# Performance work log

Hardware: AMD Instinct MI355X
Metric: run time of the kernel (lower is better)

## Reference

```python
import math
import jax, jax.numpy as jnp
import numpy as np

B, S, D, H, P, FF = 64, 100, 768, 8, 8, 3072
HD = D // H
NUM_LAYERS = 4
EPS = 1e-5


def _layernorm(x, g, b):
    m = jnp.mean(x, axis=-1, keepdims=True)
    v = jnp.mean(jnp.square(x - m), axis=-1, keepdims=True)
    return (x - m) * jax.lax.rsqrt(v + EPS) * g + b


def _positional_encoding(seq_len, d_model):
    pos = jnp.arange(seq_len, dtype=jnp.float32)[:, None]
    div = jnp.exp(jnp.arange(0, d_model, 2, dtype=jnp.float32) * (-math.log(10000.0) / d_model))
    pe = jnp.zeros((seq_len, d_model), dtype=jnp.float32)
    pe = pe.at[:, 0::2].set(jnp.sin(pos * div))
    pe = pe.at[:, 1::2].set(jnp.cos(pos * div))
    return pe[None]  # [1, S, D]


def setup_inputs() -> dict:
    key = jax.random.key(0)
    ks = jax.random.split(key, 12)
    s = 0.02
    return {
        "template_seq": jax.random.normal(ks[0], (B, S, D), jnp.float32),
        "param_seq": jax.random.normal(ks[1], (B, S, P, 768), jnp.float32),
        # ParamEncoder (shared across all 4 layers)
        "Wc": jax.random.normal(ks[2], (768, D), jnp.float32) * s,
        "bc": jnp.zeros((D,), jnp.float32),
        "gp": jnp.ones((D,), jnp.float32),
        "bp": jnp.zeros((D,), jnp.float32),
        # FFN (shared)
        "W1": jax.random.normal(ks[3], (D, FF), jnp.float32) * s,
        "b1": jnp.zeros((FF,), jnp.float32),
        "W2": jax.random.normal(ks[4], (FF, D), jnp.float32) * s,
        "b2": jnp.zeros((D,), jnp.float32),
        # LayerNorms (shared)
        "g1": jnp.ones((D,), jnp.float32),
        "bn1": jnp.zeros((D,), jnp.float32),
        "g2": jnp.ones((D,), jnp.float32),
        "bn2": jnp.zeros((D,), jnp.float32),
        # final classifier
        "Wfc": jax.random.normal(ks[5], (D * S, 2), jnp.float32) * s,
        "bfc": jnp.zeros((2,), jnp.float32),
    }


def _layer(src, param_seq, Wc, bc, gp, bp, W1, b1, W2, b2, g1, bn1, g2, bn2):
    inv_sqrt_hd = 1.0 / math.sqrt(HD)
    # ParamEncoder: Linear(768->D) per param vector, mean over params, LayerNorm.
    # Linear is linear => mean-then-project is identical to project-then-mean.
    pooled = jnp.mean(param_seq, axis=2)                  # [B, S, 768]
    param_enc = _layernorm(pooled @ Wc + bc, gp, bp)       # [B, S, D]
    pb = param_enc.reshape(B, S, H, HD).transpose(0, 2, 1, 3)  # [B, H, S, HD]
    param_bias = jnp.einsum('bhqd,bhkd->bhqk', pb, pb) * inv_sqrt_hd
    # attention with q = k = v = src (no projections in the original forward)
    q = src.reshape(B, S, H, HD).transpose(0, 2, 1, 3)     # [B, H, S, HD]
    attn = jnp.einsum('bhqd,bhkd->bhqk', q, q) * inv_sqrt_hd + param_bias
    attn = jax.nn.softmax(attn, axis=-1)
    out = jnp.einsum('bhqk,bhkd->bhqd', attn, q)
    out = out.transpose(0, 2, 1, 3).reshape(B, S, D)
    src = _layernorm(src + out, g1, bn1)
    ffn = jax.nn.gelu(src @ W1 + b1, approximate=False) @ W2 + b2
    return _layernorm(src + ffn, g2, bn2)


def reference(template_seq, param_seq, Wc, bc, gp, bp, W1, b1, W2, b2,
              g1, bn1, g2, bn2, Wfc, bfc):
    x = template_seq + _positional_encoding(S, D)
    for _ in range(NUM_LAYERS):
        x = _layer(x, param_seq, Wc, bc, gp, bp, W1, b1, W2, b2, g1, bn1, g2, bn2)
    return x.reshape(B, S * D) @ Wfc + bfc  # [B, 2]
```

## Files before the change

### kernel.cpp

```cpp
#include <hip/hip_runtime.h>
#include <hip/hip_bf16.h>
#include <math.h>


typedef __attribute__((ext_vector_type(8))) short bf16x8;
typedef __attribute__((ext_vector_type(4))) float f32x4;
typedef __attribute__((ext_vector_type(4))) short short4v;

#define BB 64
#define SS 100
#define DD 768
#define HH 8
#define HD 96
#define FF_ 3072
#define ROWS 6400
#define LN10000 9.210340371976184f

__device__ __forceinline__ void async_copy16(void* lds_dst, const void* gsrc) {
  __builtin_amdgcn_global_load_lds(
      (const __attribute__((address_space(1))) void*)gsrc,
      (__attribute__((address_space(3))) void*)lds_dst, 16, 0, 0);
}

__device__ __forceinline__ float block_sum256(float v, float* sbuf) {
#pragma unroll
  for (int o = 32; o > 0; o >>= 1) v += __shfl_xor(v, o, 64);
  int tid = threadIdx.x;
  __syncthreads();
  if ((tid & 63) == 0) sbuf[tid >> 6] = v;
  __syncthreads();
  return sbuf[0] + sbuf[1] + sbuf[2] + sbuf[3];
}

__device__ __forceinline__ float block_sum192(float v, float* sbuf) {
#pragma unroll
  for (int o = 32; o > 0; o >>= 1) v += __shfl_xor(v, o, 64);
  int tid = threadIdx.x;
  __syncthreads();
  if ((tid & 63) == 0) sbuf[tid >> 6] = v;
  __syncthreads();
  return sbuf[0] + sbuf[1] + sbuf[2];
}

__global__ void convert_transpose(const float* __restrict__ in,
                                  __hip_bfloat16* __restrict__ out,
                                  int K, int N) {
  __shared__ float t[32][33];
  int n0 = blockIdx.x * 32, k0 = blockIdx.y * 32;
  int tid = threadIdx.x;
  int tx = tid & 31, ty = tid >> 5;
#pragma unroll
  for (int j = 0; j < 32; j += 8)
    t[ty + j][tx] = in[(size_t)(k0 + ty + j) * N + n0 + tx];
  __syncthreads();
#pragma unroll
  for (int j = 0; j < 32; j += 8)
    out[(size_t)(n0 + ty + j) * K + k0 + tx] = __float2bfloat16(t[tx][ty + j]);
}

__global__ void pool_mean(const float* __restrict__ ps,
                          __hip_bfloat16* __restrict__ pooled) {
  int idx = blockIdx.x * 256 + threadIdx.x;
  int row = idx / DD, c = idx - row * DD;
  float s = 0.f;
#pragma unroll
  for (int p = 0; p < 8; p++) s += ps[(size_t)(row * 8 + p) * DD + c];
  pooled[idx] = __float2bfloat16(s * 0.125f);
}

__global__ void add_pe(const float* __restrict__ t, float* __restrict__ src) {
  int idx = blockIdx.x * 256 + threadIdx.x;
  int row = idx / DD, c = idx - row * DD;
  int srow = row % SS;
  int c2 = c & ~1;
  float ang = (float)srow * expf((float)c2 * (-LN10000 / (float)DD));
  float pe = (c & 1) ? cosf(ang) : sinf(ang);
  src[idx] = t[idx] + pe;
}

template <bool XB16, bool RESID, bool WB16>
__global__ void ln_row(const float* __restrict__ Xf,
                       const __hip_bfloat16* __restrict__ Xb,
                       const float* __restrict__ R,
                       const float* __restrict__ g, const float* __restrict__ bb,
                       float* __restrict__ of, __hip_bfloat16* __restrict__ ob) {
  int row = blockIdx.x, tid = threadIdx.x;
  size_t base = (size_t)row * DD;
  int c4 = tid * 4;
  float4 v;
  if constexpr (XB16) {
    short4v xv = *(const short4v*)(Xb + base + c4);
    __hip_bfloat16* p = (__hip_bfloat16*)&xv;
    v.x = __bfloat162float(p[0]); v.y = __bfloat162float(p[1]);
    v.z = __bfloat162float(p[2]); v.w = __bfloat162float(p[3]);
  } else {
    v = *(const float4*)(Xf + base + c4);
  }
  if (RESID) {
    float4 rv = *(const float4*)(R + base + c4);
    v.x += rv.x; v.y += rv.y; v.z += rv.z; v.w += rv.w;
  }
  __shared__ float sbuf[3];
  float s = block_sum192(v.x + v.y + v.z + v.w, sbuf);
  float mean = s * (1.0f / DD);
  float dx = v.x - mean, dy = v.y - mean, dz = v.z - mean, dw = v.w - mean;
  float ss = block_sum192(dx * dx + dy * dy + dz * dz + dw * dw, sbuf);
  float rs = rsqrtf(ss * (1.0f / DD) + 1e-5f);
  float4 gv = *(const float4*)(g + c4);
  float4 bv = *(const float4*)(bb + c4);
  float4 y;
  y.x = dx * rs * gv.x + bv.x;
  y.y = dy * rs * gv.y + bv.y;
  y.z = dz * rs * gv.z + bv.z;
  y.w = dw * rs * gv.w + bv.w;
  *(float4*)(of + base + c4) = y;
  if (WB16) {
    __hip_bfloat16 hb[4] = {__float2bfloat16(y.x), __float2bfloat16(y.y),
                            __float2bfloat16(y.z), __float2bfloat16(y.w)};
    *(short4v*)(ob + base + c4) = *(short4v*)hb;
  }
}

__launch_bounds__(256, 2)
__global__ void param_bias_mfma(const float* __restrict__ penc,
                                float* __restrict__ pbias) {
  __shared__ __align__(16) __hip_bfloat16 Qs[128][104];
  const int bh = blockIdx.x;
  const int b = bh >> 3, h = bh & 7;
  const int tid = threadIdx.x;
  const int wave = tid >> 6, lane = tid & 63;
  const int r = lane & 15, quad = lane >> 4;
  const int q8 = quad * 8;
  const int wr = (wave >> 1) * 64, wc = (wave & 1) * 64;
  const float sroot = rsqrtf(9.79795897113f);
  for (int i = tid; i < 128 * HD; i += 256) {
    int s = i / HD, d = i - s * HD;
    float v = (s < SS) ? penc[(size_t)(b * SS + s) * DD + h * HD + d] : 0.f;
    Qs[s][d] = __float2bfloat16(v * sroot);
  }
  __syncthreads();
  f32x4 acc[4][4] = {};
#pragma unroll
  for (int k0 = 0; k0 < HD; k0 += 32) {
    bf16x8 af[4], bfv[4];
#pragma unroll
    for (int mi = 0; mi < 4; mi++)
      af[mi] = *(const bf16x8*)&Qs[wr + mi * 16 + r][k0 + q8];
#pragma unroll
    for (int ni = 0; ni < 4; ni++)
      bfv[ni] = *(const bf16x8*)&Qs[wc + ni * 16 + r][k0 + q8];
#pragma unroll
    for (int mi = 0; mi < 4; mi++)
#pragma unroll
      for (int ni = 0; ni < 4; ni++)
        acc[mi][ni] = __builtin_amdgcn_mfma_f32_16x16x32_bf16(af[mi], bfv[ni],
                                                              acc[mi][ni], 0, 0, 0);
  }
  float* pb = pbias + (size_t)bh * SS * SS;
#pragma unroll
  for (int mi = 0; mi < 4; mi++)
#pragma unroll
    for (int ni = 0; ni < 4; ni++) {
      int col = wc + ni * 16 + r;
      if (col < SS) {
#pragma unroll
        for (int rg = 0; rg < 4; rg++) {
          int row = wr + mi * 16 + quad * 4 + rg;
          if (row < SS) pb[row * SS + col] = acc[mi][ni][rg];
        }
      }
    }
}

__launch_bounds__(256, 2)
__global__ void attn_fused_mfma(const float* __restrict__ src,
                                const float* __restrict__ pbias,
                                __hip_bfloat16* __restrict__ out) {
  __shared__ __align__(16) char umem[128 * 136 * 2];
  __shared__ __align__(16) __hip_bfloat16 Qt[96][136];
  __shared__ float redm[2][128];
  __shared__ float reds[2][128];
  __hip_bfloat16 (*Qs)[104] = (__hip_bfloat16 (*)[104])umem;
  __hip_bfloat16 (*Ps)[136] = (__hip_bfloat16 (*)[136])umem;

  const int bh = blockIdx.x;
  const int b = bh >> 3, h = bh & 7;
  const int tid = threadIdx.x;
  const int wave = tid >> 6, lane = tid & 63;
  const int r = lane & 15, quad = lane >> 4;
  const int q8 = quad * 8;
  const int wr = (wave >> 1) * 64, wc = (wave & 1) * 64;

  const float sroot = rsqrtf(9.79795897113f);
  for (int i = tid; i < SS * HD; i += 256) {
    int s = i / HD, d = i - s * HD;
    float v = src[(size_t)(b * SS + s) * DD + h * HD + d];
    Qs[s][d] = __float2bfloat16(v * sroot);
    Qt[d][s] = __float2bfloat16(v);
  }
  for (int i = tid; i < 28 * HD; i += 256) {
    int s = i / HD, d = i - s * HD;
    Qs[100 + s][d] = __float2bfloat16(0.f);
    Qt[d][100 + s] = __float2bfloat16(0.f);
  }

  const float* pb = pbias + (size_t)bh * SS * SS;
  bool cv[4]; int cols[4];
#pragma unroll
  for (int ni = 0; ni < 4; ni++) { cols[ni] = wc + ni * 16 + r; cv[ni] = cols[ni] < SS; }
  f32x4 acc[4][4];
#pragma unroll
  for (int mi = 0; mi < 4; mi++)
#pragma unroll
    for (int rg = 0; rg < 4; rg++) {
      int row = wr + mi * 16 + quad * 4 + rg;
#pragma unroll
      for (int ni = 0; ni < 4; ni++)
        acc[mi][ni][rg] = (row < SS && cv[ni]) ? pb[row * SS + cols[ni]] : 0.f;
    }
  __syncthreads();

#pragma unroll
  for (int k0 = 0; k0 < HD; k0 += 32) {
    bf16x8 af[4], bfv[4];
#pragma unroll
    for (int mi = 0; mi < 4; mi++)
      af[mi] = *(const bf16x8*)&Qs[wr + mi * 16 + r][k0 + q8];
#pragma unroll
    for (int ni = 0; ni < 4; ni++)
      bfv[ni] = *(const bf16x8*)&Qs[wc + ni * 16 + r][k0 + q8];
#pragma unroll
    for (int mi = 0; mi < 4; mi++)
#pragma unroll
      for (int ni = 0; ni < 4; ni++)
        acc[mi][ni] = __builtin_amdgcn_mfma_f32_16x16x32_bf16(af[mi], bfv[ni],
                                                              acc[mi][ni], 0, 0, 0);
  }

  float mx[4][4];
#pragma unroll
  for (int mi = 0; mi < 4; mi++)
#pragma unroll
    for (int rg = 0; rg < 4; rg++) {
      float m = -1e30f;
#pragma unroll
      for (int ni = 0; ni < 4; ni++)
        if (cv[ni]) m = fmaxf(m, acc[mi][ni][rg]);
#pragma unroll
      for (int o = 1; o < 16; o <<= 1) m = fmaxf(m, __shfl_xor(m, o, 64));
      mx[mi][rg] = m;
    }
  if (r == 0) {
#pragma unroll
    for (int mi = 0; mi < 4; mi++)
#pragma unroll
      for (int rg = 0; rg < 4; rg++)
        redm[wave & 1][wr + mi * 16 + quad * 4 + rg] = mx[mi][rg];
  }
  __syncthreads();

#pragma unroll
  for (int mi = 0; mi < 4; mi++)
#pragma unroll
    for (int rg = 0; rg < 4; rg++) {
      int row = wr + mi * 16 + quad * 4 + rg;
      float rmax = fmaxf(redm[0][row], redm[1][row]);
      float s = 0.f;
#pragma unroll
      for (int ni = 0; ni < 4; ni++) {
        float e = cv[ni] ? __expf(acc[mi][ni][rg] - rmax) : 0.f;
        acc[mi][ni][rg] = e;
        s += e;
      }
#pragma unroll
      for (int o = 1; o < 16; o <<= 1) s += __shfl_xor(s, o, 64);
      if (r == 0) reds[wave & 1][row] = s;
    }
  __syncthreads();

#pragma unroll
  for (int mi = 0; mi < 4; mi++)
#pragma unroll
    for (int rg = 0; rg < 4; rg++) {
      int row = wr + mi * 16 + quad * 4 + rg;
      float inv = 1.0f / (reds[0][row] + reds[1][row]);
#pragma unroll
      for (int ni = 0; ni < 4; ni++)
        Ps[row][cols[ni]] = __float2bfloat16(acc[mi][ni][rg] * inv);
    }
  __syncthreads();

  const int wr2 = (wave >> 1) * 48;
  f32x4 po[3][4] = {};
#pragma unroll
  for (int kk = 0; kk < 128; kk += 32) {
    bf16x8 aq[3], bp[4];
#pragma unroll
    for (int mi = 0; mi < 3; mi++)
      aq[mi] = *(const bf16x8*)&Qt[wr2 + mi * 16 + r][kk + q8];
#pragma unroll
    for (int ni = 0; ni < 4; ni++)
      bp[ni] = *(const bf16x8*)&Ps[wc + ni * 16 + r][kk + q8];
#pragma unroll
    for (int mi = 0; mi < 3; mi++)
#pragma unroll
      for (int ni = 0; ni < 4; ni++)
        po[mi][ni] = __builtin_amdgcn_mfma_f32_16x16x32_bf16(aq[mi], bp[ni],
                                                             po[mi][ni], 0, 0, 0);
  }
#pragma unroll
  for (int mi = 0; mi < 3; mi++)
#pragma unroll
    for (int ni = 0; ni < 4; ni++) {
      int qcol = wc + ni * 16 + r;
      if (qcol < SS) {
        int d0 = wr2 + mi * 16 + quad * 4;
        __hip_bfloat16 hb[4];
#pragma unroll
        for (int rg = 0; rg < 4; rg++) hb[rg] = __float2bfloat16(po[mi][ni][rg]);
        *(short4v*)(out + (size_t)(b * SS + qcol) * DD + h * HD + d0) = *(short4v*)hb;
      }
    }
}

template <int MODE>
__launch_bounds__(512, 4)
__global__ void gemm256(const __hip_bfloat16* __restrict__ A,
                        const __hip_bfloat16* __restrict__ Bt,
                        const float* __restrict__ bias,
                        const float* __restrict__ resid,
                        float* __restrict__ outf,
                        __hip_bfloat16* __restrict__ outb,
                        int M, int N, int K) {
  constexpr int BM = 256, BN = 128, BK = 32;
  __shared__ __align__(16) __hip_bfloat16 As[3][BM * BK];
  __shared__ __align__(16) __hip_bfloat16 Bs[3][BN * BK];
  const int gm = M >> 8, gn = N >> 7;
  const int nwg = gm * gn;
  int wg = (int)blockIdx.x;
  {
    int qc = nwg >> 3, rc = nwg & 7;
    int xcd = wg & 7, pos = wg >> 3;
    wg = (xcd < rc ? xcd * (qc + 1) : rc * (qc + 1) + (xcd - rc) * qc) + pos;
  }
  const int nt0 = wg / gm, mt = wg - nt0 * gm;
  const int m0 = mt * BM, n0 = nt0 * BN;
  const int tid = threadIdx.x;
  const int wave = tid >> 6, lane = tid & 63;
  const int wm = wave >> 1, wn = wave & 1;
  const int r = lane & 15, q = lane >> 4;

  const int srow = tid >> 2;
  const int scp = (tid & 3) ^ ((srow >> 1) & 3);
  const __hip_bfloat16* gA0 = A + (size_t)(m0 + srow) * K + scp * 8;
  const __hip_bfloat16* gA1 = A + (size_t)(m0 + srow + 128) * K + scp * 8;
  const __hip_bfloat16* gB0 = Bt + (size_t)(n0 + srow) * K + scp * 8;

  const int key8 = ((r >> 1) & 3) * 8;
  const int cq = (q * 8) ^ key8;
  const int aBase = wm * 2048 + r * 32;
  const int bBase = wn * 2048 + r * 32;

  f32x4 acc[4][4] = {};

  const int NT = K / BK;
#pragma unroll
  for (int t = 0; t < 2; ++t) {
    const int kel = t * BK;
    async_copy16(&As[t][tid * 8],          gA0 + kel);
    async_copy16(&As[t][(tid + 512) * 8],  gA1 + kel);
    async_copy16(&Bs[t][tid * 8],          gB0 + kel);
  }
  asm volatile("s_waitcnt vmcnt(3)" ::: "memory");
  __builtin_amdgcn_s_barrier();
  __builtin_amdgcn_sched_barrier(0);

  int slot = 0;
  for (int t = 0; t < NT; ++t) {
    const int s2 = (slot >= 1) ? slot - 1 : slot + 2;
    const bool st = (t + 2 < NT);
    const int kel = (t + 2) * BK;
    bf16x8 af[4], bfr[4];
#pragma unroll
    for (int mi = 0; mi < 4; mi++)
      af[mi] = *(const bf16x8*)(&As[slot][aBase + mi * 512 + cq]);
#pragma unroll
    for (int ni = 0; ni < 4; ni++)
      bfr[ni] = *(const bf16x8*)(&Bs[slot][bBase + ni * 512 + cq]);
    if (st) {
      async_copy16(&As[s2][tid * 8],         gA0 + kel);
      async_copy16(&As[s2][(tid + 512) * 8], gA1 + kel);
      async_copy16(&Bs[s2][tid * 8],         gB0 + kel);
    }
    __builtin_amdgcn_s_setprio(1);
#pragma unroll
    for (int mi = 0; mi < 4; mi++)
#pragma unroll
      for (int ni = 0; ni < 4; ni++)
        acc[mi][ni] = __builtin_amdgcn_mfma_f32_16x16x32_bf16(af[mi], bfr[ni],
                                                              acc[mi][ni], 0, 0, 0);
    __builtin_amdgcn_s_setprio(0);
    if (st) asm volatile("s_waitcnt vmcnt(3)" ::: "memory");
    else    asm volatile("s_waitcnt vmcnt(0)" ::: "memory");
    __builtin_amdgcn_s_barrier();
    __builtin_amdgcn_sched_barrier(0);
    slot = (slot == 2) ? 0 : slot + 1;
  }

#pragma unroll
  for (int mi = 0; mi < 4; mi++) {
#pragma unroll
    for (int ni = 0; ni < 4; ni++) {
      int col = n0 + wn * 64 + ni * 16 + r;
      float bv = bias[col];
#pragma unroll
      for (int rg = 0; rg < 4; rg++) {
        int row = m0 + wm * 64 + mi * 16 + q * 4 + rg;
        size_t oidx = (size_t)row * N + col;
        float v = acc[mi][ni][rg] + bv;
        if constexpr (MODE == 2) v += resid[oidx];
        if constexpr (MODE == 1) {
          v = 0.5f * v * (1.0f + erff(v * 0.70710678118654752f));
          outb[oidx] = __float2bfloat16(v);
        } else {
          outf[oidx] = v;
        }
      }
    }
  }
}

#define CCHUNK 3072
#define NCHUNK 25
__global__ void classifier_part(const float* __restrict__ x,
                                const float* __restrict__ Wfc,
                                float* __restrict__ part) {
  int chunk = blockIdx.x, b = blockIdx.y, tid = threadIdx.x;
  const float* xb = x + (size_t)b * (SS * DD) + chunk * CCHUNK;
  const float* w = Wfc + 2 * (size_t)chunk * CCHUNK;
  float a0 = 0.f, a1 = 0.f;
  for (int i = tid; i < CCHUNK; i += 256) {
    float xv = xb[i];
    float2 wv = *(const float2*)(w + 2 * i);
    a0 += xv * wv.x;
    a1 += xv * wv.y;
  }
  __shared__ float sbuf[4];
  a0 = block_sum256(a0, sbuf);
  a1 = block_sum256(a1, sbuf);
  if (tid == 0) {
    part[(b * NCHUNK + chunk) * 2] = a0;
    part[(b * NCHUNK + chunk) * 2 + 1] = a1;
  }
}

__global__ void classifier_final(const float* __restrict__ part,
                                 const float* __restrict__ bfc,
                                 float* __restrict__ out) {
  int b = threadIdx.x;
  float a0 = bfc[0], a1 = bfc[1];
#pragma unroll
  for (int c = 0; c < NCHUNK; c++) {
    a0 += part[(b * NCHUNK + c) * 2];
    a1 += part[(b * NCHUNK + c) * 2 + 1];
  }
  out[2 * b] = a0;
  out[2 * b + 1] = a1;
}

extern "C" void kernel_launch(void* const* d_in, const int* in_sizes, int n_in,
                              void* d_out, int out_size, void* d_ws, size_t ws_size,
                              hipStream_t stream) {
  const float* Tmpl = (const float*)d_in[0];
  const float* Pseq = (const float*)d_in[1];
  const float* Wc   = (const float*)d_in[2];
  const float* bc   = (const float*)d_in[3];
  const float* gp   = (const float*)d_in[4];
  const float* bp   = (const float*)d_in[5];
  const float* W1   = (const float*)d_in[6];
  const float* b1   = (const float*)d_in[7];
  const float* W2   = (const float*)d_in[8];
  const float* b2   = (const float*)d_in[9];
  const float* g1   = (const float*)d_in[10];
  const float* bn1  = (const float*)d_in[11];
  const float* g2   = (const float*)d_in[12];
  const float* bn2  = (const float*)d_in[13];
  const float* Wfc  = (const float*)d_in[14];
  const float* bfc  = (const float*)d_in[15];
  float* out = (float*)d_out;
  (void)in_sizes; (void)n_in; (void)out_size; (void)ws_size;

  char* ws = (char*)d_ws;
  size_t off = 0;
  auto alloc = [&](size_t n) { size_t o = off; off += (n + 255) & ~(size_t)255; return o; };

  __hip_bfloat16* Wct = (__hip_bfloat16*)(ws + alloc((size_t)768 * 768 * 2));
  __hip_bfloat16* W1t = (__hip_bfloat16*)(ws + alloc((size_t)768 * 3072 * 2));
  __hip_bfloat16* W2t = (__hip_bfloat16*)(ws + alloc((size_t)3072 * 768 * 2));
  size_t h1_off = alloc((size_t)ROWS * FF_ * 2);
  __hip_bfloat16* h1 = (__hip_bfloat16*)(ws + h1_off);
  float* param_enc = (float*)(ws + h1_off);
  size_t slb_off = alloc((size_t)ROWS * DD * 2);
  __hip_bfloat16* src_ln_bf = (__hip_bfloat16*)(ws + slb_off);
  __hip_bfloat16* pooled = (__hip_bfloat16*)(ws + slb_off);
  size_t ao_off = alloc((size_t)ROWS * DD * 4);
  __hip_bfloat16* attn_out_b = (__hip_bfloat16*)(ws + ao_off);
  float* pe_lin = (float*)(ws + ao_off);
  float* pbias = (float*)(ws + alloc((size_t)512 * SS * SS * 4));
  float* src = (float*)(ws + alloc((size_t)ROWS * DD * 4));
  float* src_ln = (float*)(ws + alloc((size_t)ROWS * DD * 4));
  float* z = (float*)(ws + alloc((size_t)ROWS * DD * 4));
  float* cpart = (float*)(ws + alloc((size_t)BB * NCHUNK * 2 * 4));

  convert_transpose<<<dim3(768 / 32, 768 / 32), 256, 0, stream>>>(Wc, Wct, 768, 768);
  convert_transpose<<<dim3(3072 / 32, 768 / 32), 256, 0, stream>>>(W1, W1t, 768, 3072);
  convert_transpose<<<dim3(768 / 32, 3072 / 32), 256, 0, stream>>>(W2, W2t, 3072, 768);
  pool_mean<<<ROWS * DD / 256, 256, 0, stream>>>(Pseq, pooled);
  gemm256<0><<<(DD / 128) * (ROWS / 256), 512, 0, stream>>>(
      pooled, Wct, bc, nullptr, pe_lin, nullptr, ROWS, DD, 768);
  ln_row<false, false, false><<<ROWS, 192, 0, stream>>>(
      pe_lin, nullptr, nullptr, gp, bp, param_enc, nullptr);
  param_bias_mfma<<<512, 256, 0, stream>>>(param_enc, pbias);
  add_pe<<<ROWS * DD / 256, 256, 0, stream>>>(Tmpl, src);

  for (int l = 0; l < 4; ++l) {
    attn_fused_mfma<<<512, 256, 0, stream>>>(src, pbias, attn_out_b);
    ln_row<true, true, true><<<ROWS, 192, 0, stream>>>(
        nullptr, attn_out_b, src, g1, bn1, src_ln, src_ln_bf);
    gemm256<1><<<(FF_ / 128) * (ROWS / 256), 512, 0, stream>>>(
        src_ln_bf, W1t, b1, nullptr, nullptr, h1, ROWS, FF_, DD);
    gemm256<2><<<(DD / 128) * (ROWS / 256), 512, 0, stream>>>(
        h1, W2t, b2, src_ln, z, nullptr, ROWS, DD, FF_);
    ln_row<false, false, false><<<ROWS, 192, 0, stream>>>(
        z, nullptr, nullptr, g2, bn2, src, nullptr);
  }

  classifier_part<<<dim3(NCHUNK, BB), 256, 0, stream>>>(src, Wfc, cpart);
  classifier_final<<<1, 64, 0, stream>>>(cpart, bfc, out);
}
```

Measured before the change: 978.0 us.

## Swap GEMM tile to 128x256, vectorize elementwise kernels, single-pass layernorm

The GEMM tile changes from 256x128 to 128x256, with the wave layout becoming 2x4 and the second async load row moving from A to B. pool_mean, add_pe and the attention Q staging now use float4 loads, and positional encodings are precomputed once into a table. LayerNorm reduces sum and sum of squares in a single paired reduction, removing one block barrier round. The single-pass E[x^2]-mean^2 variance can lose precision, and the GEMM epilogue indexing (not shown) must match the new wave mapping.

New measurement: 952.1 us. 2.7% less time.

```diff
diff --git a/kernel.cpp b/kernel.cpp
--- a/kernel.cpp
+++ b/kernel.cpp
@@ -32,14 +32,23 @@
   return sbuf[0] + sbuf[1] + sbuf[2] + sbuf[3];
 }
 
-__device__ __forceinline__ float block_sum192(float v, float* sbuf) {
-#pragma unroll
-  for (int o = 32; o > 0; o >>= 1) v += __shfl_xor(v, o, 64);
+__device__ __forceinline__ void block_sum192_pair(float v1, float v2,
+                                                  float* sbuf,
+                                                  float& S1, float& S2) {
+#pragma unroll
+  for (int o = 32; o > 0; o >>= 1) {
+    v1 += __shfl_xor(v1, o, 64);
+    v2 += __shfl_xor(v2, o, 64);
+  }
   int tid = threadIdx.x;
   __syncthreads();
-  if ((tid & 63) == 0) sbuf[tid >> 6] = v;
-  __syncthreads();
-  return sbuf[0] + sbuf[1] + sbuf[2];
+  if ((tid & 63) == 0) {
+    sbuf[2 * (tid >> 6)] = v1;
+    sbuf[2 * (tid >> 6) + 1] = v2;
+  }
+  __syncthreads();
+  S1 = sbuf[0] + sbuf[2] + sbuf[4];
+  S2 = sbuf[1] + sbuf[3] + sbuf[5];
 }
 
 __global__ void convert_transpose(const float* __restrict__ in,
@@ -60,22 +69,37 @@
 
 __global__ void pool_mean(const float* __restrict__ ps,
                           __hip_bfloat16* __restrict__ pooled) {
+  int idx4 = blockIdx.x * 256 + threadIdx.x;
+  int row = idx4 / 192, c4 = (idx4 - row * 192) * 4;
+  float4 s = {0.f, 0.f, 0.f, 0.f};
+#pragma unroll
+  for (int p = 0; p < 8; p++) {
+    float4 v = *(const float4*)(ps + (size_t)(row * 8 + p) * DD + c4);
+    s.x += v.x; s.y += v.y; s.z += v.z; s.w += v.w;
+  }
+  __hip_bfloat16 hb[4] = {__float2bfloat16(s.x * 0.125f), __float2bfloat16(s.y * 0.125f),
+                          __float2bfloat16(s.z * 0.125f), __float2bfloat16(s.w * 0.125f)};
+  *(short4v*)(pooled + (size_t)row * DD + c4) = *(short4v*)hb;
+}
+
+__global__ void pe_build(float* __restrict__ pet) {
   int idx = blockIdx.x * 256 + threadIdx.x;
-  int row = idx / DD, c = idx - row * DD;
-  float s = 0.f;
-#pragma unroll
-  for (int p = 0; p < 8; p++) s += ps[(size_t)(row * 8 + p) * DD + c];
-  pooled[idx] = __float2bfloat16(s * 0.125f);
-}
-
-__global__ void add_pe(const float* __restrict__ t, float* __restrict__ src) {
-  int idx = blockIdx.x * 256 + threadIdx.x;
-  int row = idx / DD, c = idx - row * DD;
-  int srow = row % SS;
+  if (idx >= SS * DD) return;
+  int srow = idx / DD, c = idx - srow * DD;
   int c2 = c & ~1;
   float ang = (float)srow * expf((float)c2 * (-LN10000 / (float)DD));
-  float pe = (c & 1) ? cosf(ang) : sinf(ang);
-  src[idx] = t[idx] + pe;
+  pet[idx] = (c & 1) ? cosf(ang) : sinf(ang);
+}
+
+__global__ void add_pe(const float* __restrict__ t, const float* __restrict__ pet,
+                       float* __restrict__ src) {
+  int idx4 = blockIdx.x * 256 + threadIdx.x;
+  int row = idx4 / 192, c4 = (idx4 - row * 192) * 4;
+  int srow = row % SS;
+  float4 tv = *(const float4*)(t + (size_t)row * DD + c4);
+  float4 pv = *(const float4*)(pet + (size_t)srow * DD + c4);
+  tv.x += pv.x; tv.y += pv.y; tv.z += pv.z; tv.w += pv.w;
+  *(float4*)(src + (size_t)row * DD + c4) = tv;
 }
 
 template <bool XB16, bool RESID, bool WB16>
@@ -100,12 +124,15 @@
     float4 rv = *(const float4*)(R + base + c4);
     v.x += rv.x; v.y += rv.y; v.z += rv.z; v.w += rv.w;
   }
-  __shared__ float sbuf[3];
-  float s = block_sum192(v.x + v.y + v.z + v.w, sbuf);
-  float mean = s * (1.0f / DD);
+  __shared__ float sbuf[6];
+  float S1, S2;
+  block_sum192_pair(v.x + v.y + v.z + v.w,
+                    v.x * v.x + v.y * v.y + v.z * v.z + v.w * v.w,
+                    sbuf, S1, S2);
+  float mean = S1 * (1.0f / DD);
+  float var = S2 * (1.0f / DD) - mean * mean;
+  float rs = rsqrtf(var + 1e-5f);
   float dx = v.x - mean, dy = v.y - mean, dz = v.z - mean, dw = v.w - mean;
-  float ss = block_sum192(dx * dx + dy * dy + dz * dz + dw * dw, sbuf);
-  float rs = rsqrtf(ss * (1.0f / DD) + 1e-5f);
   float4 gv = *(const float4*)(g + c4);
   float4 bv = *(const float4*)(bb + c4);
   float4 y;
@@ -192,16 +219,29 @@
   const int wr = (wave >> 1) * 64, wc = (wave & 1) * 64;
 
   const float sroot = rsqrtf(9.79795897113f);
-  for (int i = tid; i < SS * HD; i += 256) {
-    int s = i / HD, d = i - s * HD;
-    float v = src[(size_t)(b * SS + s) * DD + h * HD + d];
-    Qs[s][d] = __float2bfloat16(v * sroot);
-    Qt[d][s] = __float2bfloat16(v);
-  }
-  for (int i = tid; i < 28 * HD; i += 256) {
-    int s = i / HD, d = i - s * HD;
-    Qs[100 + s][d] = __float2bfloat16(0.f);
-    Qt[d][100 + s] = __float2bfloat16(0.f);
+  for (int i = tid; i < SS * (HD / 4); i += 256) {
+    int s = i / 24, j = i - s * 24;
+    float4 v4 = *(const float4*)(src + (size_t)(b * SS + s) * DD + h * HD + j * 4);
+    __hip_bfloat16 hb[4] = {__float2bfloat16(v4.x * sroot), __float2bfloat16(v4.y * sroot),
+                            __float2bfloat16(v4.z * sroot), __float2bfloat16(v4.w * sroot)};
+    *(short4v*)&Qs[s][j * 4] = *(short4v*)hb;
+    Qt[j * 4 + 0][s] = __float2bfloat16(v4.x);
+    Qt[j * 4 + 1][s] = __float2bfloat16(v4.y);
+    Qt[j * 4 + 2][s] = __float2bfloat16(v4.z);
+    Qt[j * 4 + 3][s] = __float2bfloat16(v4.w);
+  }
+  {
+    __hip_bfloat16 zb[4] = {__float2bfloat16(0.f), __float2bfloat16(0.f),
+                            __float2bfloat16(0.f), __float2bfloat16(0.f)};
+    short4v z4 = *(short4v*)zb;
+    for (int i = tid; i < 28 * 24; i += 256) {
+      int s = i / 24, j = i - s * 24;
+      *(short4v*)&Qs[100 + s][j * 4] = z4;
+    }
+    for (int i = tid; i < 96 * 7; i += 256) {
+      int d = i / 7, j = i - d * 7;
+      *(short4v*)&Qt[d][100 + j * 4] = z4;
+    }
   }
 
   const float* pb = pbias + (size_t)bh * SS * SS;
@@ -332,10 +372,10 @@
                         float* __restrict__ outf,
                         __hip_bfloat16* __restrict__ outb,
                         int M, int N, int K) {
-  constexpr int BM = 256, BN = 128, BK = 32;
+  constexpr int BM = 128, BN = 256, BK = 32;
   __shared__ __align__(16) __hip_bfloat16 As[3][BM * BK];
   __shared__ __align__(16) __hip_bfloat16 Bs[3][BN * BK];
-  const int gm = M >> 8, gn = N >> 7;
+  const int gm = M >> 7, gn = N >> 8;
   const int nwg = gm * gn;
   int wg = (int)blockIdx.x;
   {
@@ -347,14 +387,14 @@
   const int m0 = mt * BM, n0 = nt0 * BN;
   const int tid = threadIdx.x;
   const int wave = tid >> 6, lane = tid & 63;
-  const int wm = wave >> 1, wn = wave & 1;
+  const int wm = wave >> 2, wn = wave & 3;
   const int r = lane & 15, q = lane >> 4;
 
   const int srow = tid >> 2;
   const int scp = (tid & 3) ^ ((srow >> 1) & 3);
   const __hip_bfloat16* gA0 = A + (size_t)(m0 + srow) * K + scp * 8;
-  const __hip_bfloat16* gA1 = A + (size_t)(m0 + srow + 128) * K + scp * 8;
   const __hip_bfloat16* gB0 = Bt + (size_t)(n0 + srow) * K + scp * 8;
+  const __hip_bfloat16* gB1 = Bt + (size_t)(n0 + srow + 128) * K + scp * 8;
 
   const int key8 = ((r >> 1) & 3) * 8;
   const int cq = (q * 8) ^ key8;
@@ -368,8 +408,8 @@
   for (int t = 0; t < 2; ++t) {
     const int kel = t * BK;
     async_copy16(&As[t][tid * 8],          gA0 + kel);
-    async_copy16(&As[t][(tid + 512) * 8],  gA1 + kel);
     async_copy16(&Bs[t][tid * 8],          gB0 + kel);
+    async_copy16(&Bs[t][(tid + 512) * 8],  gB1 + kel);
   }
   asm volatile("s_waitcnt vmcnt(3)" ::: "memory");
   __builtin_amdgcn_s_barrier();
@@ -389,8 +429,8 @@
       bfr[ni] = *(const bf16x8*)(&Bs[slot][bBase + ni * 512 + cq]);
     if (st) {
       async_copy16(&As[s2][tid * 8],         gA0 + kel);
-      async_copy16(&As[s2][(tid + 512) * 8], gA1 + kel);
       async_copy16(&Bs[s2][tid * 8],         gB0 + kel);
+      async_copy16(&Bs[s2][(tid + 512) * 8], gB1 + kel);
     }
     __builtin_amdgcn_s_setprio(1);
 #pragma unroll
@@ -511,25 +551,27 @@
   float* src_ln = (float*)(ws + alloc((size_t)ROWS * DD * 4));
   float* z = (float*)(ws + alloc((size_t)ROWS * DD * 4));
   float* cpart = (float*)(ws + alloc((size_t)BB * NCHUNK * 2 * 4));
+  float* pet = (float*)(ws + alloc((size_t)SS * DD * 4));
 
   convert_transpose<<<dim3(768 / 32, 768 / 32), 256, 0, stream>>>(Wc, Wct, 768, 768);
   convert_transpose<<<dim3(3072 / 32, 768 / 32), 256, 0, stream>>>(W1, W1t, 768, 3072);
   convert_transpose<<<dim3(768 / 32, 3072 / 32), 256, 0, stream>>>(W2, W2t, 3072, 768);
-  pool_mean<<<ROWS * DD / 256, 256, 0, stream>>>(Pseq, pooled);
-  gemm256<0><<<(DD / 128) * (ROWS / 256), 512, 0, stream>>>(
+  pe_build<<<(SS * DD + 255) / 256, 256, 0, stream>>>(pet);
+  pool_mean<<<ROWS * DD / 4 / 256, 256, 0, stream>>>(Pseq, pooled);
+  gemm256<0><<<(DD / 256) * (ROWS / 128), 512, 0, stream>>>(
       pooled, Wct, bc, nullptr, pe_lin, nullptr, ROWS, DD, 768);
   ln_row<false, false, false><<<ROWS, 192, 0, stream>>>(
       pe_lin, nullptr, nullptr, gp, bp, param_enc, nullptr);
   param_bias_mfma<<<512, 256, 0, stream>>>(param_enc, pbias);
-  add_pe<<<ROWS * DD / 256, 256, 0, stream>>>(Tmpl, src);
+  add_pe<<<ROWS * DD / 4 / 256, 256, 0, stream>>>(Tmpl, pet, src);
 
   for (int l = 0; l < 4; ++l) {
     attn_fused_mfma<<<512, 256, 0, stream>>>(src, pbias, attn_out_b);
     ln_row<true, true, true><<<ROWS, 192, 0, stream>>>(
         nullptr, attn_out_b, src, g1, bn1, src_ln, src_ln_bf);
-    gemm256<1><<<(FF_ / 128) * (ROWS / 256), 512, 0, stream>>>(
+    gemm256<1><<<(FF_ / 256) * (ROWS / 128), 512, 0, stream>>>(
         src_ln_bf, W1t, b1, nullptr, nullptr, h1, ROWS, FF_, DD);
-    gemm256<2><<<(DD / 128) * (ROWS / 256), 512, 0, stream>>>(
+    gemm256<2><<<(DD / 256) * (ROWS / 128), 512, 0, stream>>>(
         h1, W2t, b2, src_ln, z, nullptr, ROWS, DD, FF_);
     ln_row<false, false, false><<<ROWS, 192, 0, stream>>>(
         z, nullptr, nullptr, g2, bn2, src, nullptr);
```
